# Optimization experiments

Measured on AMD Instinct MI355X. Metric: run time of the kernel, lower is better.

## Reference

```python
import jax, jax.numpy as jnp
import numpy as np

N_NODES = 50000
N_EDGES = 800000
ND = 64   # node_dim
HD = 128  # hidden_dim
ED = 32   # edge_dim


def setup_inputs() -> dict:
    key = jax.random.key(0)
    ks = jax.random.split(key, 16)
    init = lambda k, shape: (jax.random.normal(k, shape, jnp.float32)
                             / np.float32(np.sqrt(shape[0])))
    h = jax.random.normal(ks[0], (N_NODES, ND), jnp.float32)
    x = jax.random.normal(ks[1], (N_NODES, 3), jnp.float32) * 10.0
    edge_index = jax.random.randint(ks[2], (2, N_EDGES), 0, N_NODES, dtype=jnp.int64)
    # realistic edge distances = actual pairwise distances of sampled edges
    edge_dist = jnp.linalg.norm(x[edge_index[0]] - x[edge_index[1]], axis=-1)
    in_dim = 2 * ND + ED
    return {
        "h": h, "x": x, "edge_index": edge_index, "edge_dist": edge_dist,
        # edge_mlp: Linear(1, ED) -> SiLU -> Linear(ED, ED)
        "We1": init(ks[3], (1, ED)), "be1": jnp.zeros((ED,), jnp.float32),
        "We2": init(ks[4], (ED, ED)), "be2": jnp.zeros((ED,), jnp.float32),
        # node_mlp: Linear(in_dim, HD) -> SiLU -> Linear(HD, ND)
        "Wn1": init(ks[5], (in_dim, HD)), "bn1": jnp.zeros((HD,), jnp.float32),
        "Wn2": init(ks[6], (HD, ND)), "bn2": jnp.zeros((ND,), jnp.float32),
        # coord_mlp: Linear(in_dim, HD) -> SiLU -> Linear(HD, 1, bias=False)
        "Wc1": init(ks[7], (in_dim, HD)), "bc1": jnp.zeros((HD,), jnp.float32),
        "Wc2": init(ks[8], (HD, 1)),
    }


def reference(h, x, edge_index, edge_dist,
              We1, be1, We2, be2,
              Wn1, bn1, Wn2, bn2,
              Wc1, bc1, Wc2):
    n = h.shape[0]
    src, dst = edge_index[0], edge_index[1]
    # edge_mlp on scalar distance -> [E, ED]
    e = jax.nn.silu(edge_dist[:, None] @ We1 + be1) @ We2 + be2
    # gather + concat -> [E, 2*ND + ED]
    m_input = jnp.concatenate([h[src], h[dst], e], axis=-1)
    # node messages [E, ND]
    m = jax.nn.silu(m_input @ Wn1 + bn1) @ Wn2 + bn2
    h_agg = jax.ops.segment_sum(m, dst, num_segments=n)
    # coord update weight [E, 1]
    coord_weight = jax.nn.silu(m_input @ Wc1 + bc1) @ Wc2
    dir_vec = x[src] - x[dst]
    dir_len = jnp.clip(jnp.linalg.norm(dir_vec, axis=-1, keepdims=True), 1e-8)
    coord_update = coord_weight * (dir_vec / dir_len)
    x_agg = jax.ops.segment_sum(coord_update, dst, num_segments=n)
    return h + h_agg, x + x_agg
```

## Files before the change

### kernel.cpp

```cpp
#include <hip/hip_runtime.h>


#define NN 50000
#define NE 800000
#define NDIM 64
#define HDIM 128
#define NTILES (NE / 64)
#define MSTRIDE 168
#define HSTRIDE 136
#define NH (NN * NDIM)
#define NX (NN * 3)

#define WS_HBF    0
#define WS_WN1P   6400000
#define WS_WC1P   6440960
#define WS_BN1P   6481920
#define WS_BC1P   6482432

typedef __bf16 bf16x8 __attribute__((ext_vector_type(8)));
typedef float f32x4 __attribute__((ext_vector_type(4)));
typedef unsigned short ushort8 __attribute__((ext_vector_type(8)));
typedef unsigned short ushort4v __attribute__((ext_vector_type(4)));

__device__ __forceinline__ unsigned short f2bf(float f) {
    union { float f; unsigned int u; } c; c.f = f;
    unsigned int r = c.u + 0x7fffu + ((c.u >> 16) & 1u);
    return (unsigned short)(r >> 16);
}
__device__ __forceinline__ unsigned int pk2bf(float a, float b) {
    return (unsigned int)f2bf(a) | ((unsigned int)f2bf(b) << 16);
}
__device__ __forceinline__ float silu(float v) {
    return v * __builtin_amdgcn_rcpf(1.0f + __expf(-v));
}
__device__ __forceinline__ bf16x8 ld_frag(const unsigned short* p) {
    union { ushort8 u; bf16x8 v; } c;
    c.u = *(const ushort8*)p;
    return c.v;
}
__device__ __forceinline__ bf16x8 mk_frag(const unsigned short* u) {
    union { ushort8 uu; bf16x8 v; } c;
#pragma unroll
    for (int j = 0; j < 8; ++j) c.uu[j] = u[j];
    return c.v;
}

__global__ void init_out(const float* __restrict__ h, const float* __restrict__ x,
                         float* __restrict__ out) {
    int i = blockIdx.x * 256 + threadIdx.x;
    if (i < NH) out[i] = h[i];
    else if (i < NH + NX) out[i] = x[i - NH];
}

__global__ void prep_h(const float* __restrict__ h, unsigned short* __restrict__ hbf) {
    int i = (blockIdx.x * 256 + threadIdx.x) * 4;
    if (i < NH) {
        float4 v = *(const float4*)(h + i);
        ushort4v u = { f2bf(v.x), f2bf(v.y), f2bf(v.z), f2bf(v.w) };
        *(ushort4v*)(hbf + i) = u;
    }
}

__global__ void prep_w(const float* __restrict__ We2, const float* __restrict__ be2,
                       const float* __restrict__ Wn1, const float* __restrict__ bn1,
                       const float* __restrict__ Wc1, const float* __restrict__ bc1,
                       unsigned short* __restrict__ wn1p, unsigned short* __restrict__ wc1p,
                       float* __restrict__ bn1p, float* __restrict__ bc1p) {
    int idx = blockIdx.x * 256 + threadIdx.x;
    if (idx >= 160 * 128) return;
    int k = idx >> 7, n = idx & 127;
    float vn, vc;
    if (k < 128) {
        vn = Wn1[k * HDIM + n];
        vc = Wc1[k * HDIM + n];
    } else {
        int i = k - 128;
        float sn = 0.0f, sc = 0.0f;
        for (int j = 0; j < 32; ++j) {
            float w = We2[i * 32 + j];
            sn += w * Wn1[(128 + j) * HDIM + n];
            sc += w * Wc1[(128 + j) * HDIM + n];
        }
        vn = sn; vc = sc;
    }
    wn1p[idx] = f2bf(vn);
    wc1p[idx] = f2bf(vc);
    if (idx < 128) {
        float sn = bn1[idx], sc = bc1[idx];
        for (int j = 0; j < 32; ++j) {
            sn += be2[j] * Wn1[(128 + j) * HDIM + idx];
            sc += be2[j] * Wc1[(128 + j) * HDIM + idx];
        }
        bn1p[idx] = sn;
        bc1p[idx] = sc;
    }
}

__global__ __launch_bounds__(256, 2) void egnn_edges(
    const unsigned short* __restrict__ hbf, const float* __restrict__ x,
    const int* __restrict__ srcg, const int* __restrict__ dstg,
    const float* __restrict__ dist,
    const float* __restrict__ We1, const float* __restrict__ be1,
    const unsigned short* __restrict__ wn1p, const float* __restrict__ bn1p,
    const float* __restrict__ Wn2, const float* __restrict__ bn2,
    const unsigned short* __restrict__ wc1p, const float* __restrict__ bc1p,
    const float* __restrict__ Wc2,
    float* __restrict__ outh, float* __restrict__ outx) {

    __shared__ __align__(16) unsigned short mlds[64 * MSTRIDE];
    __shared__ __align__(16) unsigned short hl[64 * HSTRIDE];
    __shared__ int src_l[64];
    __shared__ int dst_l[64];
    __shared__ float dist_l[64];
    __shared__ float part_l[256];

    const int tid  = threadIdx.x;
    const int w    = tid >> 6;
    const int lane = tid & 63;
    const int l15  = lane & 15;
    const int quad = lane >> 4;

    bf16x8 wn1f[5][2], wc1f[5][2];
#pragma unroll
    for (int kc = 0; kc < 5; ++kc) {
#pragma unroll
        for (int nt = 0; nt < 2; ++nt) {
            unsigned short un[8], uc[8];
            const int n = w * 32 + l15 * 2 + nt;
#pragma unroll
            for (int j = 0; j < 8; ++j) {
                const int k = kc * 32 + quad * 8 + j;
                un[j] = wn1p[k * HDIM + n];
                uc[j] = wc1p[k * HDIM + n];
            }
            wn1f[kc][nt] = mk_frag(un);
            wc1f[kc][nt] = mk_frag(uc);
        }
    }
    bf16x8 wn2f[4];
#pragma unroll
    for (int kc = 0; kc < 4; ++kc) {
        unsigned short u[8];
        const int n = w * 16 + l15;
#pragma unroll
        for (int j = 0; j < 8; ++j) {
            const int k = kc * 32 + quad * 8 + j;
            u[j] = f2bf(Wn2[k * NDIM + n]);
        }
        wn2f[kc] = mk_frag(u);
    }
    const float biasN0 = bn1p[w * 32 + l15 * 2];
    const float biasN1 = bn1p[w * 32 + l15 * 2 + 1];
    const float biasC0 = bc1p[w * 32 + l15 * 2];
    const float biasC1 = bc1p[w * 32 + l15 * 2 + 1];
    const float bias2v = bn2[w * 16 + l15];
    const float wc2a = Wc2[w * 32 + l15 * 2];
    const float wc2b = Wc2[w * 32 + l15 * 2 + 1];

    for (int tile = blockIdx.x; tile < NTILES; tile += gridDim.x) {
        __syncthreads();

        if (tid < 64) {
            const int e = tile * 64 + tid;
            src_l[tid] = srcg[e];
            dst_l[tid] = dstg[e];
            dist_l[tid] = dist[e];
        }
        __syncthreads();

        {
            const int c8 = tid & 7, sub = tid >> 3;
#pragma unroll
            for (int it = 0; it < 2; ++it) {
                const int el = sub + it * 32;
                const ushort8 hs = *(const ushort8*)(hbf + (size_t)src_l[el] * NDIM + c8 * 8);
                const ushort8 hd = *(const ushort8*)(hbf + (size_t)dst_l[el] * NDIM + c8 * 8);
                *(ushort8*)&mlds[el * MSTRIDE + c8 * 8] = hs;
                *(ushort8*)&mlds[el * MSTRIDE + 64 + c8 * 8] = hd;
            }
        }
        {
            const float dv = dist_l[lane];
            ushort8 su;
#pragma unroll
            for (int j = 0; j < 8; ++j) {
                const int k = w * 8 + j;
                su[j] = f2bf(silu(fmaf(dv, We1[k], be1[k])));
            }
            *(ushort8*)&mlds[lane * MSTRIDE + 128 + w * 8] = su;
        }
        __syncthreads();

        f32x4 accN[4][2], accC[4][2];
#pragma unroll
        for (int mt = 0; mt < 4; ++mt) {
            accN[mt][0] = (f32x4){biasN0, biasN0, biasN0, biasN0};
            accN[mt][1] = (f32x4){biasN1, biasN1, biasN1, biasN1};
            accC[mt][0] = (f32x4){biasC0, biasC0, biasC0, biasC0};
            accC[mt][1] = (f32x4){biasC1, biasC1, biasC1, biasC1};
        }
#pragma unroll
        for (int kc = 0; kc < 5; ++kc) {
            bf16x8 af[4];
#pragma unroll
            for (int mt = 0; mt < 4; ++mt)
                af[mt] = ld_frag(&mlds[(mt * 16 + l15) * MSTRIDE + kc * 32 + quad * 8]);
#pragma unroll
            for (int mt = 0; mt < 4; ++mt) {
#pragma unroll
                for (int nt = 0; nt < 2; ++nt) {
                    accN[mt][nt] = __builtin_amdgcn_mfma_f32_16x16x32_bf16(
                        af[mt], wn1f[kc][nt], accN[mt][nt], 0, 0, 0);
                    accC[mt][nt] = __builtin_amdgcn_mfma_f32_16x16x32_bf16(
                        af[mt], wc1f[kc][nt], accC[mt][nt], 0, 0, 0);
                }
            }
        }

#pragma unroll
        for (int mt = 0; mt < 4; ++mt) {
#pragma unroll
            for (int r = 0; r < 4; ++r) {
                const int row = mt * 16 + quad * 4 + r;
                *(unsigned int*)&hl[row * HSTRIDE + w * 32 + l15 * 2] =
                    pk2bf(silu(accN[mt][0][r]), silu(accN[mt][1][r]));
            }
        }
        __syncthreads();

        f32x4 acc2[4];
#pragma unroll
        for (int mt = 0; mt < 4; ++mt) acc2[mt] = (f32x4){bias2v, bias2v, bias2v, bias2v};
#pragma unroll
        for (int kc = 0; kc < 4; ++kc) {
#pragma unroll
            for (int mt = 0; mt < 4; ++mt) {
                bf16x8 a2 = ld_frag(&hl[(mt * 16 + l15) * HSTRIDE + kc * 32 + quad * 8]);
                acc2[mt] = __builtin_amdgcn_mfma_f32_16x16x32_bf16(a2, wn2f[kc], acc2[mt], 0, 0, 0);
            }
        }
#pragma unroll
        for (int mt = 0; mt < 4; ++mt) {
#pragma unroll
            for (int r = 0; r < 4; ++r) {
                const int el = mt * 16 + quad * 4 + r;
                atomicAdd(outh + (size_t)dst_l[el] * NDIM + w * 16 + l15, acc2[mt][r]);
            }
        }

        {
            float vals[16];
#pragma unroll
            for (int mt = 0; mt < 4; ++mt)
#pragma unroll
                for (int r = 0; r < 4; ++r)
                    vals[mt * 4 + r] = silu(accC[mt][0][r]) * wc2a +
                                       silu(accC[mt][1][r]) * wc2b;
#pragma unroll
            for (int m = 8; m >= 1; m >>= 1) {
                const bool up = (l15 & m) != 0;
#pragma unroll
                for (int j = 0; j < 8; ++j) {
                    if (j < m) {
                        float send = up ? vals[j] : vals[j + m];
                        float recv = __shfl_xor(send, m, 64);
                        vals[j] = (up ? vals[j + m] : vals[j]) + recv;
                    }
                }
            }
            const int edge = ((l15 >> 2) << 4) + (quad << 2) + (l15 & 3);
            part_l[w * 64 + edge] = vals[0];
        }
        __syncthreads();

        if (tid < 64) {
            const float cw = part_l[tid] + part_l[64 + tid] + part_l[128 + tid] + part_l[192 + tid];
            const int sn = src_l[tid], dn = dst_l[tid];
            const float dx = x[sn * 3 + 0] - x[dn * 3 + 0];
            const float dy = x[sn * 3 + 1] - x[dn * 3 + 1];
            const float dz = x[sn * 3 + 2] - x[dn * 3 + 2];
            float len = sqrtf(dx * dx + dy * dy + dz * dz);
            len = fmaxf(len, 1e-8f);
            const float f = cw / len;
            atomicAdd(outx + (size_t)dn * 3 + 0, f * dx);
            atomicAdd(outx + (size_t)dn * 3 + 1, f * dy);
            atomicAdd(outx + (size_t)dn * 3 + 2, f * dz);
        }
    }
}

extern "C" void kernel_launch(void* const* d_in, const int* in_sizes, int n_in,
                              void* d_out, int out_size, void* d_ws, size_t ws_size,
                              hipStream_t stream) {
    const float* h    = (const float*)d_in[0];
    const float* x    = (const float*)d_in[1];
    const int*   ei   = (const int*)d_in[2];
    const float* dist = (const float*)d_in[3];
    const float* We1  = (const float*)d_in[4];
    const float* be1  = (const float*)d_in[5];
    const float* We2  = (const float*)d_in[6];
    const float* be2  = (const float*)d_in[7];
    const float* Wn1  = (const float*)d_in[8];
    const float* bn1  = (const float*)d_in[9];
    const float* Wn2  = (const float*)d_in[10];
    const float* bn2  = (const float*)d_in[11];
    const float* Wc1  = (const float*)d_in[12];
    const float* bc1  = (const float*)d_in[13];
    const float* Wc2  = (const float*)d_in[14];

    unsigned short* hbf  = (unsigned short*)((char*)d_ws + WS_HBF);
    unsigned short* wn1p = (unsigned short*)((char*)d_ws + WS_WN1P);
    unsigned short* wc1p = (unsigned short*)((char*)d_ws + WS_WC1P);
    float* bn1p = (float*)((char*)d_ws + WS_BN1P);
    float* bc1p = (float*)((char*)d_ws + WS_BC1P);

    float* outh = (float*)d_out;
    float* outx = outh + (size_t)NH;

    prep_h<<<(NH / 4 + 255) / 256, 256, 0, stream>>>(h, hbf);
    prep_w<<<(160 * 128 + 255) / 256, 256, 0, stream>>>(We2, be2, Wn1, bn1, Wc1, bc1,
                                                        wn1p, wc1p, bn1p, bc1p);
    init_out<<<(NH + NX + 255) / 256, 256, 0, stream>>>(h, x, (float*)d_out);
    egnn_edges<<<512, 256, 0, stream>>>(hbf, x, ei, ei + NE, dist,
                                        We1, be1, wn1p, bn1p,
                                        Wn2, bn2, wc1p, bc1p, Wc2,
                                        outh, outx);
}
```

Before: 450.1 us.

## Double-buffer edge tiles, prefetch next gathers, fuse prep kernels, drop coord reduction barrier

Merges the three prep kernels into one launch that copies h/x to the output and converts h to bf16 in the same pass. The edge kernel now double-buffers the LDS message tile, issuing the next tile's index, distance and h gathers during the current tile's MFMA work, and replaces __syncthreads with a raw lgkmcnt wait plus barrier. Unit direction vectors are precomputed one tile ahead, and each wave atomically adds its partial coordinate contribution directly instead of reducing through LDS. This trades extra LDS, registers and four times as many coord atomics for fewer barriers and hidden gather latency.

Result: slower. 810.3 us (+80.0%).

```diff
diff --git a/kernel.cpp b/kernel.cpp
--- a/kernel.cpp
+++ b/kernel.cpp
@@ -11,17 +11,19 @@
 #define NH (NN * NDIM)
 #define NX (NN * 3)
 
-#define WS_HBF    0
-#define WS_WN1P   6400000
-#define WS_WC1P   6440960
-#define WS_BN1P   6481920
-#define WS_BC1P   6482432
+#define WS_HBF   0
+#define WS_WN1P  6400000
+#define WS_WC1P  6440960
+#define WS_BN1P  6481920
+#define WS_BC1P  6482432
 
 typedef __bf16 bf16x8 __attribute__((ext_vector_type(8)));
 typedef float f32x4 __attribute__((ext_vector_type(4)));
 typedef unsigned short ushort8 __attribute__((ext_vector_type(8)));
 typedef unsigned short ushort4v __attribute__((ext_vector_type(4)));
 
+#define LGKM_BARRIER() asm volatile("s_waitcnt lgkmcnt(0)\n\ts_barrier" ::: "memory")
+
 __device__ __forceinline__ unsigned short f2bf(float f) {
     union { float f; unsigned int u; } c; c.f = f;
     unsigned int r = c.u + 0x7fffu + ((c.u >> 16) & 1u);
@@ -45,54 +47,52 @@
     return c.v;
 }
 
-__global__ void init_out(const float* __restrict__ h, const float* __restrict__ x,
-                         float* __restrict__ out) {
-    int i = blockIdx.x * 256 + threadIdx.x;
-    if (i < NH) out[i] = h[i];
-    else if (i < NH + NX) out[i] = x[i - NH];
-}
-
-__global__ void prep_h(const float* __restrict__ h, unsigned short* __restrict__ hbf) {
-    int i = (blockIdx.x * 256 + threadIdx.x) * 4;
-    if (i < NH) {
-        float4 v = *(const float4*)(h + i);
-        ushort4v u = { f2bf(v.x), f2bf(v.y), f2bf(v.z), f2bf(v.w) };
-        *(ushort4v*)(hbf + i) = u;
-    }
-}
-
-__global__ void prep_w(const float* __restrict__ We2, const float* __restrict__ be2,
-                       const float* __restrict__ Wn1, const float* __restrict__ bn1,
-                       const float* __restrict__ Wc1, const float* __restrict__ bc1,
-                       unsigned short* __restrict__ wn1p, unsigned short* __restrict__ wc1p,
-                       float* __restrict__ bn1p, float* __restrict__ bc1p) {
-    int idx = blockIdx.x * 256 + threadIdx.x;
-    if (idx >= 160 * 128) return;
-    int k = idx >> 7, n = idx & 127;
-    float vn, vc;
-    if (k < 128) {
-        vn = Wn1[k * HDIM + n];
-        vc = Wc1[k * HDIM + n];
-    } else {
-        int i = k - 128;
-        float sn = 0.0f, sc = 0.0f;
-        for (int j = 0; j < 32; ++j) {
-            float w = We2[i * 32 + j];
-            sn += w * Wn1[(128 + j) * HDIM + n];
-            sc += w * Wc1[(128 + j) * HDIM + n];
-        }
-        vn = sn; vc = sc;
-    }
-    wn1p[idx] = f2bf(vn);
-    wc1p[idx] = f2bf(vc);
-    if (idx < 128) {
-        float sn = bn1[idx], sc = bc1[idx];
-        for (int j = 0; j < 32; ++j) {
-            sn += be2[j] * Wn1[(128 + j) * HDIM + idx];
-            sc += be2[j] * Wc1[(128 + j) * HDIM + idx];
-        }
-        bn1p[idx] = sn;
-        bc1p[idx] = sc;
+__global__ void prep_all(
+    const float* __restrict__ h, const float* __restrict__ x,
+    const float* __restrict__ We2, const float* __restrict__ be2,
+    const float* __restrict__ Wn1, const float* __restrict__ bn1,
+    const float* __restrict__ Wc1, const float* __restrict__ bc1,
+    float* __restrict__ out, unsigned short* __restrict__ hbf,
+    unsigned short* __restrict__ wn1p, unsigned short* __restrict__ wc1p,
+    float* __restrict__ bn1p, float* __restrict__ bc1p) {
+    int gid = blockIdx.x * 256 + threadIdx.x;
+    if (gid < 837500) {
+        if (gid < 800000) {
+            float4 v = ((const float4*)h)[gid];
+            ((float4*)out)[gid] = v;
+            ushort4v u = { f2bf(v.x), f2bf(v.y), f2bf(v.z), f2bf(v.w) };
+            ((ushort4v*)hbf)[gid] = u;
+        } else {
+            ((float4*)out)[gid] = ((const float4*)x)[gid - 800000];
+        }
+    } else if (gid < 837500 + 20480) {
+        int idx = gid - 837500;
+        int k = idx >> 7, n = idx & 127;
+        float vn, vc;
+        if (k < 128) {
+            vn = Wn1[k * HDIM + n];
+            vc = Wc1[k * HDIM + n];
+        } else {
+            int i = k - 128;
+            float sn = 0.0f, sc = 0.0f;
+            for (int j = 0; j < 32; ++j) {
+                float wv = We2[i * 32 + j];
+                sn += wv * Wn1[(128 + j) * HDIM + n];
+                sc += wv * Wc1[(128 + j) * HDIM + n];
+            }
+            vn = sn; vc = sc;
+        }
+        wn1p[idx] = f2bf(vn);
+        wc1p[idx] = f2bf(vc);
+        if (idx < 128) {
+            float sn = bn1[idx], sc = bc1[idx];
+            for (int j = 0; j < 32; ++j) {
+                sn += be2[j] * Wn1[(128 + j) * HDIM + idx];
+                sc += be2[j] * Wc1[(128 + j) * HDIM + idx];
+            }
+            bn1p[idx] = sn;
+            bc1p[idx] = sc;
+        }
     }
 }
 
@@ -107,34 +107,35 @@
     const float* __restrict__ Wc2,
     float* __restrict__ outh, float* __restrict__ outx) {
 
-    __shared__ __align__(16) unsigned short mlds[64 * MSTRIDE];
+    __shared__ __align__(16) unsigned short mlds[2][64 * MSTRIDE];
     __shared__ __align__(16) unsigned short hl[64 * HSTRIDE];
-    __shared__ int src_l[64];
-    __shared__ int dst_l[64];
-    __shared__ float dist_l[64];
-    __shared__ float part_l[256];
+    __shared__ int dst_l[2][64];
+    __shared__ float4 unit_l[2][64];
 
     const int tid  = threadIdx.x;
     const int w    = tid >> 6;
     const int lane = tid & 63;
     const int l15  = lane & 15;
     const int quad = lane >> 4;
+    const int c8   = tid & 7;
+    const int sub  = tid >> 3;
+    const int bedge = ((l15 >> 2) << 4) + (quad << 2) + (l15 & 3);
 
     bf16x8 wn1f[5][2], wc1f[5][2];
 #pragma unroll
     for (int kc = 0; kc < 5; ++kc) {
 #pragma unroll
         for (int nt = 0; nt < 2; ++nt) {
-            unsigned short un[8], uc[8];
+            unsigned short un_[8], uc_[8];
             const int n = w * 32 + l15 * 2 + nt;
 #pragma unroll
             for (int j = 0; j < 8; ++j) {
                 const int k = kc * 32 + quad * 8 + j;
-                un[j] = wn1p[k * HDIM + n];
-                uc[j] = wc1p[k * HDIM + n];
-            }
-            wn1f[kc][nt] = mk_frag(un);
-            wc1f[kc][nt] = mk_frag(uc);
+                un_[j] = wn1p[k * HDIM + n];
+                uc_[j] = wc1p[k * HDIM + n];
+            }
+            wn1f[kc][nt] = mk_frag(un_);
+            wc1f[kc][nt] = mk_frag(uc_);
         }
     }
     bf16x8 wn2f[4];
@@ -148,6 +149,12 @@
             u[j] = f2bf(Wn2[k * NDIM + n]);
         }
         wn2f[kc] = mk_frag(u);
+    }
+    float we1r[8], be1r[8];
+#pragma unroll
+    for (int j = 0; j < 8; ++j) {
+        we1r[j] = We1[w * 8 + j];
+        be1r[j] = be1[w * 8 + j];
     }
     const float biasN0 = bn1p[w * 32 + l15 * 2];
     const float biasN1 = bn1p[w * 32 + l15 * 2 + 1];
@@ -157,39 +164,46 @@
     const float wc2a = Wc2[w * 32 + l15 * 2];
     const float wc2b = Wc2[w * 32 + l15 * 2 + 1];
 
-    for (int tile = blockIdx.x; tile < NTILES; tile += gridDim.x) {
-        __syncthreads();
-
+    const int t0 = blockIdx.x;
+    const int gstep = (int)gridDim.x;
+    {
+        const int sA = srcg[t0 * 64 + sub], sB = srcg[t0 * 64 + sub + 32];
+        const int dA = dstg[t0 * 64 + sub], dB = dstg[t0 * 64 + sub + 32];
+        const float dv = dist[t0 * 64 + lane];
+        const ushort8 hsa = *(const ushort8*)(hbf + sA * NDIM + c8 * 8);
+        const ushort8 hda = *(const ushort8*)(hbf + dA * NDIM + c8 * 8);
+        const ushort8 hsb = *(const ushort8*)(hbf + sB * NDIM + c8 * 8);
+        const ushort8 hdb = *(const ushort8*)(hbf + dB * NDIM + c8 * 8);
+        *(ushort8*)&mlds[0][sub * MSTRIDE + c8 * 8] = hsa;
+        *(ushort8*)&mlds[0][sub * MSTRIDE + 64 + c8 * 8] = hda;
+        *(ushort8*)&mlds[0][(sub + 32) * MSTRIDE + c8 * 8] = hsb;
+        *(ushort8*)&mlds[0][(sub + 32) * MSTRIDE + 64 + c8 * 8] = hdb;
+        ushort8 su;
+#pragma unroll
+        for (int j = 0; j < 8; ++j)
+            su[j] = f2bf(silu(fmaf(dv, we1r[j], be1r[j])));
+        *(ushort8*)&mlds[0][lane * MSTRIDE + 128 + w * 8] = su;
+        if (c8 == 0) { dst_l[0][sub] = dA; dst_l[0][sub + 32] = dB; }
         if (tid < 64) {
-            const int e = tile * 64 + tid;
-            src_l[tid] = srcg[e];
-            dst_l[tid] = dstg[e];
-            dist_l[tid] = dist[e];
-        }
-        __syncthreads();
-
-        {
-            const int c8 = tid & 7, sub = tid >> 3;
-#pragma unroll
-            for (int it = 0; it < 2; ++it) {
-                const int el = sub + it * 32;
-                const ushort8 hs = *(const ushort8*)(hbf + (size_t)src_l[el] * NDIM + c8 * 8);
-                const ushort8 hd = *(const ushort8*)(hbf + (size_t)dst_l[el] * NDIM + c8 * 8);
-                *(ushort8*)&mlds[el * MSTRIDE + c8 * 8] = hs;
-                *(ushort8*)&mlds[el * MSTRIDE + 64 + c8 * 8] = hd;
-            }
-        }
-        {
-            const float dv = dist_l[lane];
-            ushort8 su;
-#pragma unroll
-            for (int j = 0; j < 8; ++j) {
-                const int k = w * 8 + j;
-                su[j] = f2bf(silu(fmaf(dv, We1[k], be1[k])));
-            }
-            *(ushort8*)&mlds[lane * MSTRIDE + 128 + w * 8] = su;
-        }
-        __syncthreads();
+            const int us = srcg[t0 * 64 + tid], ud = dstg[t0 * 64 + tid];
+            const float ddx = x[us * 3 + 0] - x[ud * 3 + 0];
+            const float ddy = x[us * 3 + 1] - x[ud * 3 + 1];
+            const float ddz = x[us * 3 + 2] - x[ud * 3 + 2];
+            const float len = fmaxf(sqrtf(ddx * ddx + ddy * ddy + ddz * ddz), 1e-8f);
+            const float inv = __builtin_amdgcn_rcpf(len);
+            unit_l[0][tid] = make_float4(ddx * inv, ddy * inv, ddz * inv, 0.0f);
+        }
+    }
+
+    int p = 0;
+    for (int tile = t0; tile < NTILES; tile += gstep) {
+        const int tnx = tile + gstep;
+        const int tc = (tnx < NTILES) ? tnx : tile;
+        const int nsA = srcg[tc * 64 + sub], nsB = srcg[tc * 64 + sub + 32];
+        const int ndA = dstg[tc * 64 + sub], ndB = dstg[tc * 64 + sub + 32];
+        const float ndv = dist[tc * 64 + lane];
+
+        LGKM_BARRIER();
 
         f32x4 accN[4][2], accC[4][2];
 #pragma unroll
@@ -204,7 +218,7 @@
             bf16x8 af[4];
 #pragma unroll
             for (int mt = 0; mt < 4; ++mt)
-                af[mt] = ld_frag(&mlds[(mt * 16 + l15) * MSTRIDE + kc * 32 + quad * 8]);
+                af[mt] = ld_frag(&mlds[p][(mt * 16 + l15) * MSTRIDE + kc * 32 + quad * 8]);
 #pragma unroll
             for (int mt = 0; mt < 4; ++mt) {
 #pragma unroll
@@ -217,6 +231,11 @@
             }
         }
 
+        const ushort8 ghsa = *(const ushort8*)(hbf + nsA * NDIM + c8 * 8);
+        const ushort8 ghda = *(const ushort8*)(hbf + ndA * NDIM + c8 * 8);
+        const ushort8 ghsb = *(const ushort8*)(hbf + nsB * NDIM + c8 * 8);
+        const ushort8 ghdb = *(const ushort8*)(hbf + ndB * NDIM + c8 * 8);
+
 #pragma unroll
         for (int mt = 0; mt < 4; ++mt) {
 #pragma unroll
@@ -226,7 +245,7 @@
                     pk2bf(silu(accN[mt][0][r]), silu(accN[mt][1][r]));
             }
         }
-        __syncthreads();
+        LGKM_BARRIER();
 
         f32x4 acc2[4];
 #pragma unroll
@@ -244,7 +263,7 @@
 #pragma unroll
             for (int r = 0; r < 4; ++r) {
                 const int el = mt * 16 + quad * 4 + r;
-                atomicAdd(outh + (size_t)dst_l[el] * NDIM + w * 16 + l15, acc2[mt][r]);
+                atomicAdd(outh + dst_l[p][el] * NDIM + w * 16 + l15, acc2[mt][r]);
             }
         }
 
@@ -268,24 +287,36 @@
                     }
                 }
             }
-            const int edge = ((l15 >> 2) << 4) + (quad << 2) + (l15 & 3);
-            part_l[w * 64 + edge] = vals[0];
-        }
-        __syncthreads();
-
+            const float4 un = unit_l[p][bedge];
+            const int dn = dst_l[p][bedge];
+            const float cwp = vals[0];
+            atomicAdd(outx + dn * 3 + 0, cwp * un.x);
+            atomicAdd(outx + dn * 3 + 1, cwp * un.y);
+            atomicAdd(outx + dn * 3 + 2, cwp * un.z);
+        }
+
+        *(ushort8*)&mlds[p ^ 1][sub * MSTRIDE + c8 * 8] = ghsa;
+        *(ushort8*)&mlds[p ^ 1][sub * MSTRIDE + 64 + c8 * 8] = ghda;
+        *(ushort8*)&mlds[p ^ 1][(sub + 32) * MSTRIDE + c8 * 8] = ghsb;
+        *(ushort8*)&mlds[p ^ 1][(sub + 32) * MSTRIDE + 64 + c8 * 8] = ghdb;
+        {
+            ushort8 su;
+#pragma unroll
+            for (int j = 0; j < 8; ++j)
+                su[j] = f2bf(silu(fmaf(ndv, we1r[j], be1r[j])));
+            *(ushort8*)&mlds[p ^ 1][lane * MSTRIDE + 128 + w * 8] = su;
+        }
+        if (c8 == 0) { dst_l[p ^ 1][sub] = ndA; dst_l[p ^ 1][sub + 32] = ndB; }
         if (tid < 64) {
-            const float cw = part_l[tid] + part_l[64 + tid] + part_l[128 + tid] + part_l[192 + tid];
-            const int sn = src_l[tid], dn = dst_l[tid];
-            const float dx = x[sn * 3 + 0] - x[dn * 3 + 0];
-            const float dy = x[sn * 3 + 1] - x[dn * 3 + 1];
-            const float dz = x[sn * 3 + 2] - x[dn * 3 + 2];
-            float len = sqrtf(dx * dx + dy * dy + dz * dz);
-            len = fmaxf(len, 1e-8f);
-            const float f = cw / len;
-            atomicAdd(outx + (size_t)dn * 3 + 0, f * dx);
-            atomicAdd(outx + (size_t)dn * 3 + 1, f * dy);
-            atomicAdd(outx + (size_t)dn * 3 + 2, f * dz);
-        }
+            const int us = srcg[tc * 64 + tid], ud = dstg[tc * 64 + tid];
+            const float ddx = x[us * 3 + 0] - x[ud * 3 + 0];
+            const float ddy = x[us * 3 + 1] - x[ud * 3 + 1];
+            const float ddz = x[us * 3 + 2] - x[ud * 3 + 2];
+            const float len = fmaxf(sqrtf(ddx * ddx + ddy * ddy + ddz * ddz), 1e-8f);
+            const float inv = __builtin_amdgcn_rcpf(len);
+            unit_l[p ^ 1][tid] = make_float4(ddx * inv, ddy * inv, ddz * inv, 0.0f);
+        }
+        p ^= 1;
     }
 }
 
@@ -317,10 +348,10 @@
     float* outh = (float*)d_out;
     float* outx = outh + (size_t)NH;
 
-    prep_h<<<(NH / 4 + 255) / 256, 256, 0, stream>>>(h, hbf);
-    prep_w<<<(160 * 128 + 255) / 256, 256, 0, stream>>>(We2, be2, Wn1, bn1, Wc1, bc1,
-                                                        wn1p, wc1p, bn1p, bc1p);
-    init_out<<<(NH + NX + 255) / 256, 256, 0, stream>>>(h, x, (float*)d_out);
+    const int prep_items = 837500 + 20480;
+    prep_all<<<(prep_items + 255) / 256, 256, 0, stream>>>(
+        h, x, We2, be2, Wn1, bn1, Wc1, bc1,
+        (float*)d_out, hbf, wn1p, wc1p, bn1p, bc1p);
     egnn_edges<<<512, 256, 0, stream>>>(hbf, x, ei, ei + NE, dist,
                                         We1, be1, wn1p, bn1p,
                                         Wn2, bn2, wc1p, bc1p, Wc2,
```

## Bucket edges by destination and reduce messages in shared memory

Applied to the files above, without the earlier changes.

Adds a counting-sort pipeline (histogram, single-block scan, scatter) that groups edges into buckets of 16 destination nodes. The edge kernel then processes one bucket per block iteration and accumulates node and coordinate messages in shared-memory atomics, writing each node's result once instead of issuing global float atomics per edge. The three prep kernels are also merged into one, and We1/be1 are hoisted into registers. The cost is extra prep passes over all edges, global atomics in the scatter, and partially filled 64-edge tiles at bucket ends. Because the scatter order is nondeterministic, the summation order, and so the floating-point results, can vary slightly between runs.

After: 811.2 us. 80.2% more time.

```diff
diff --git a/kernel.cpp b/kernel.cpp
--- a/kernel.cpp
+++ b/kernel.cpp
@@ -5,17 +5,22 @@
 #define NE 800000
 #define NDIM 64
 #define HDIM 128
-#define NTILES (NE / 64)
+#define NBUCK 3125
 #define MSTRIDE 168
 #define HSTRIDE 136
 #define NH (NN * NDIM)
 #define NX (NN * 3)
 
 #define WS_HBF    0
-#define WS_WN1P   6400000
-#define WS_WC1P   6440960
-#define WS_BN1P   6481920
-#define WS_BC1P   6482432
+#define WS_SRCS   6400000
+#define WS_DSTS   9600000
+#define WS_DISTS  12800000
+#define WS_WN1P   16000000
+#define WS_WC1P   16040960
+#define WS_BN1P   16081920
+#define WS_BC1P   16082432
+#define WS_START  16082944
+#define WS_CURS   16095448
 
 typedef __bf16 bf16x8 __attribute__((ext_vector_type(8)));
 typedef float f32x4 __attribute__((ext_vector_type(4)));
@@ -45,61 +50,105 @@
     return c.v;
 }
 
-__global__ void init_out(const float* __restrict__ h, const float* __restrict__ x,
-                         float* __restrict__ out) {
-    int i = blockIdx.x * 256 + threadIdx.x;
-    if (i < NH) out[i] = h[i];
-    else if (i < NH + NX) out[i] = x[i - NH];
-}
-
-__global__ void prep_h(const float* __restrict__ h, unsigned short* __restrict__ hbf) {
-    int i = (blockIdx.x * 256 + threadIdx.x) * 4;
-    if (i < NH) {
-        float4 v = *(const float4*)(h + i);
-        ushort4v u = { f2bf(v.x), f2bf(v.y), f2bf(v.z), f2bf(v.w) };
-        *(ushort4v*)(hbf + i) = u;
-    }
-}
-
-__global__ void prep_w(const float* __restrict__ We2, const float* __restrict__ be2,
-                       const float* __restrict__ Wn1, const float* __restrict__ bn1,
-                       const float* __restrict__ Wc1, const float* __restrict__ bc1,
-                       unsigned short* __restrict__ wn1p, unsigned short* __restrict__ wc1p,
-                       float* __restrict__ bn1p, float* __restrict__ bc1p) {
-    int idx = blockIdx.x * 256 + threadIdx.x;
-    if (idx >= 160 * 128) return;
-    int k = idx >> 7, n = idx & 127;
-    float vn, vc;
-    if (k < 128) {
-        vn = Wn1[k * HDIM + n];
-        vc = Wc1[k * HDIM + n];
-    } else {
-        int i = k - 128;
-        float sn = 0.0f, sc = 0.0f;
-        for (int j = 0; j < 32; ++j) {
-            float w = We2[i * 32 + j];
-            sn += w * Wn1[(128 + j) * HDIM + n];
-            sc += w * Wc1[(128 + j) * HDIM + n];
-        }
-        vn = sn; vc = sc;
-    }
-    wn1p[idx] = f2bf(vn);
-    wc1p[idx] = f2bf(vc);
-    if (idx < 128) {
-        float sn = bn1[idx], sc = bc1[idx];
-        for (int j = 0; j < 32; ++j) {
-            sn += be2[j] * Wn1[(128 + j) * HDIM + idx];
-            sc += be2[j] * Wc1[(128 + j) * HDIM + idx];
-        }
-        bn1p[idx] = sn;
-        bc1p[idx] = sc;
+__global__ void prep_all(
+    const float* __restrict__ h, const float* __restrict__ x,
+    const float* __restrict__ We2, const float* __restrict__ be2,
+    const float* __restrict__ Wn1, const float* __restrict__ bn1,
+    const float* __restrict__ Wc1, const float* __restrict__ bc1,
+    float* __restrict__ out, unsigned short* __restrict__ hbf,
+    unsigned short* __restrict__ wn1p, unsigned short* __restrict__ wc1p,
+    float* __restrict__ bn1p, float* __restrict__ bc1p, int* __restrict__ hist) {
+    int gid = blockIdx.x * 256 + threadIdx.x;
+    if (gid < 837500) {
+        if (gid < 800000) {
+            float4 v = ((const float4*)h)[gid];
+            ((float4*)out)[gid] = v;
+            ushort4v u = { f2bf(v.x), f2bf(v.y), f2bf(v.z), f2bf(v.w) };
+            ((ushort4v*)hbf)[gid] = u;
+        } else {
+            ((float4*)out)[gid] = ((const float4*)x)[gid - 800000];
+        }
+    } else if (gid < 837500 + 20480) {
+        int idx = gid - 837500;
+        int k = idx >> 7, n = idx & 127;
+        float vn, vc;
+        if (k < 128) {
+            vn = Wn1[k * HDIM + n];
+            vc = Wc1[k * HDIM + n];
+        } else {
+            int i = k - 128;
+            float sn = 0.0f, sc = 0.0f;
+            for (int j = 0; j < 32; ++j) {
+                float wv = We2[i * 32 + j];
+                sn += wv * Wn1[(128 + j) * HDIM + n];
+                sc += wv * Wc1[(128 + j) * HDIM + n];
+            }
+            vn = sn; vc = sc;
+        }
+        wn1p[idx] = f2bf(vn);
+        wc1p[idx] = f2bf(vc);
+        if (idx < 128) {
+            float sn = bn1[idx], sc = bc1[idx];
+            for (int j = 0; j < 32; ++j) {
+                sn += be2[j] * Wn1[(128 + j) * HDIM + idx];
+                sc += be2[j] * Wc1[(128 + j) * HDIM + idx];
+            }
+            bn1p[idx] = sn;
+            bc1p[idx] = sc;
+        }
+    } else if (gid < 837500 + 20480 + NBUCK + 1) {
+        hist[gid - (837500 + 20480)] = 0;
+    }
+}
+
+__global__ void prep_hist(const int* __restrict__ dstg, int* __restrict__ hist) {
+    int e = blockIdx.x * 256 + threadIdx.x;
+    if (e < NE) atomicAdd(&hist[dstg[e] >> 4], 1);
+}
+
+__global__ void prep_scan(int* curs, int* start) {
+    __shared__ int sd[256];
+    __shared__ int carry_s;
+    const int tid = threadIdx.x;
+    if (tid == 0) carry_s = 0;
+    __syncthreads();
+    for (int c = 0; c < 13; ++c) {
+        const int i = c * 256 + tid;
+        const int v = (i < NBUCK) ? curs[i] : 0;
+        sd[tid] = v;
+        __syncthreads();
+        for (int off = 1; off < 256; off <<= 1) {
+            int t = (tid >= off) ? sd[tid - off] : 0;
+            __syncthreads();
+            sd[tid] += t;
+            __syncthreads();
+        }
+        const int excl = sd[tid] - v + carry_s;
+        if (i <= NBUCK) { start[i] = excl; curs[i] = excl; }
+        __syncthreads();
+        if (tid == 0) carry_s += sd[255];
+        __syncthreads();
+    }
+}
+
+__global__ void prep_scatter(const int* __restrict__ srcg, const int* __restrict__ dstg,
+                             const float* __restrict__ dist, int* __restrict__ curs,
+                             int* __restrict__ src_s, int* __restrict__ dst_s,
+                             float* __restrict__ dist_s) {
+    int e = blockIdx.x * 256 + threadIdx.x;
+    if (e < NE) {
+        int d = dstg[e];
+        int pos = atomicAdd(&curs[d >> 4], 1);
+        src_s[pos] = srcg[e];
+        dst_s[pos] = d;
+        dist_s[pos] = dist[e];
     }
 }
 
 __global__ __launch_bounds__(256, 2) void egnn_edges(
     const unsigned short* __restrict__ hbf, const float* __restrict__ x,
-    const int* __restrict__ srcg, const int* __restrict__ dstg,
-    const float* __restrict__ dist,
+    const int* __restrict__ src_s, const int* __restrict__ dst_s,
+    const float* __restrict__ dist_s, const int* __restrict__ start,
     const float* __restrict__ We1, const float* __restrict__ be1,
     const unsigned short* __restrict__ wn1p, const float* __restrict__ bn1p,
     const float* __restrict__ Wn2, const float* __restrict__ bn2,
@@ -109,6 +158,8 @@
 
     __shared__ __align__(16) unsigned short mlds[64 * MSTRIDE];
     __shared__ __align__(16) unsigned short hl[64 * HSTRIDE];
+    __shared__ __align__(16) float nodeacc[16][68];
+    __shared__ float xacc[16][3];
     __shared__ int src_l[64];
     __shared__ int dst_l[64];
     __shared__ float dist_l[64];
@@ -119,22 +170,23 @@
     const int lane = tid & 63;
     const int l15  = lane & 15;
     const int quad = lane >> 4;
+    const int bedge = ((l15 >> 2) << 4) + (quad << 2) + (l15 & 3);
 
     bf16x8 wn1f[5][2], wc1f[5][2];
 #pragma unroll
     for (int kc = 0; kc < 5; ++kc) {
 #pragma unroll
         for (int nt = 0; nt < 2; ++nt) {
-            unsigned short un[8], uc[8];
+            unsigned short un_[8], uc_[8];
             const int n = w * 32 + l15 * 2 + nt;
 #pragma unroll
             for (int j = 0; j < 8; ++j) {
                 const int k = kc * 32 + quad * 8 + j;
-                un[j] = wn1p[k * HDIM + n];
-                uc[j] = wc1p[k * HDIM + n];
-            }
-            wn1f[kc][nt] = mk_frag(un);
-            wc1f[kc][nt] = mk_frag(uc);
+                un_[j] = wn1p[k * HDIM + n];
+                uc_[j] = wc1p[k * HDIM + n];
+            }
+            wn1f[kc][nt] = mk_frag(un_);
+            wc1f[kc][nt] = mk_frag(uc_);
         }
     }
     bf16x8 wn2f[4];
@@ -148,6 +200,12 @@
             u[j] = f2bf(Wn2[k * NDIM + n]);
         }
         wn2f[kc] = mk_frag(u);
+    }
+    float we1r[8], be1r[8];
+#pragma unroll
+    for (int j = 0; j < 8; ++j) {
+        we1r[j] = We1[w * 8 + j];
+        be1r[j] = be1[w * 8 + j];
     }
     const float biasN0 = bn1p[w * 32 + l15 * 2];
     const float biasN1 = bn1p[w * 32 + l15 * 2 + 1];
@@ -157,135 +215,160 @@
     const float wc2a = Wc2[w * 32 + l15 * 2];
     const float wc2b = Wc2[w * 32 + l15 * 2 + 1];
 
-    for (int tile = blockIdx.x; tile < NTILES; tile += gridDim.x) {
+    for (int b = blockIdx.x; b < NBUCK; b += gridDim.x) {
+        const int base_node = b << 4;
+        const int e_start = start[b];
+        const int e_end = start[b + 1];
+
+        for (int i = tid; i < 16 * 68; i += 256) ((float*)nodeacc)[i] = 0.0f;
+        if (tid < 48) ((float*)xacc)[tid] = 0.0f;
+
+        for (int e0 = e_start; e0 < e_end; e0 += 64) {
+            const int cnt = min(64, e_end - e0);
+            __syncthreads();
+
+            if (tid < 64) {
+                const int ee = e0 + ((tid < cnt) ? tid : (cnt - 1));
+                src_l[tid] = src_s[ee];
+                dst_l[tid] = dst_s[ee];
+                dist_l[tid] = dist_s[ee];
+            }
+            __syncthreads();
+
+            {
+                const int c8 = tid & 7, sub = tid >> 3;
+#pragma unroll
+                for (int it = 0; it < 2; ++it) {
+                    const int el = sub + it * 32;
+                    const ushort8 hs = *(const ushort8*)(hbf + src_l[el] * NDIM + c8 * 8);
+                    const ushort8 hd = *(const ushort8*)(hbf + dst_l[el] * NDIM + c8 * 8);
+                    *(ushort8*)&mlds[el * MSTRIDE + c8 * 8] = hs;
+                    *(ushort8*)&mlds[el * MSTRIDE + 64 + c8 * 8] = hd;
+                }
+            }
+            {
+                const float dv = dist_l[lane];
+                ushort8 su;
+#pragma unroll
+                for (int j = 0; j < 8; ++j)
+                    su[j] = f2bf(silu(fmaf(dv, we1r[j], be1r[j])));
+                *(ushort8*)&mlds[lane * MSTRIDE + 128 + w * 8] = su;
+            }
+            __syncthreads();
+
+            f32x4 accN[4][2], accC[4][2];
+#pragma unroll
+            for (int mt = 0; mt < 4; ++mt) {
+                accN[mt][0] = (f32x4){biasN0, biasN0, biasN0, biasN0};
+                accN[mt][1] = (f32x4){biasN1, biasN1, biasN1, biasN1};
+                accC[mt][0] = (f32x4){biasC0, biasC0, biasC0, biasC0};
+                accC[mt][1] = (f32x4){biasC1, biasC1, biasC1, biasC1};
+            }
+#pragma unroll
+            for (int kc = 0; kc < 5; ++kc) {
+                bf16x8 af[4];
+#pragma unroll
+                for (int mt = 0; mt < 4; ++mt)
+                    af[mt] = ld_frag(&mlds[(mt * 16 + l15) * MSTRIDE + kc * 32 + quad * 8]);
+#pragma unroll
+                for (int mt = 0; mt < 4; ++mt) {
+#pragma unroll
+                    for (int nt = 0; nt < 2; ++nt) {
+                        accN[mt][nt] = __builtin_amdgcn_mfma_f32_16x16x32_bf16(
+                            af[mt], wn1f[kc][nt], accN[mt][nt], 0, 0, 0);
+                        accC[mt][nt] = __builtin_amdgcn_mfma_f32_16x16x32_bf16(
+                            af[mt], wc1f[kc][nt], accC[mt][nt], 0, 0, 0);
+                    }
+                }
+            }
+
+#pragma unroll
+            for (int mt = 0; mt < 4; ++mt) {
+#pragma unroll
+                for (int r = 0; r < 4; ++r) {
+                    const int row = mt * 16 + quad * 4 + r;
+                    *(unsigned int*)&hl[row * HSTRIDE + w * 32 + l15 * 2] =
+                        pk2bf(silu(accN[mt][0][r]), silu(accN[mt][1][r]));
+                }
+            }
+            __syncthreads();
+
+            f32x4 acc2[4];
+#pragma unroll
+            for (int mt = 0; mt < 4; ++mt) acc2[mt] = (f32x4){bias2v, bias2v, bias2v, bias2v};
+#pragma unroll
+            for (int kc = 0; kc < 4; ++kc) {
+#pragma unroll
+                for (int mt = 0; mt < 4; ++mt) {
+                    bf16x8 a2 = ld_frag(&hl[(mt * 16 + l15) * HSTRIDE + kc * 32 + quad * 8]);
+                    acc2[mt] = __builtin_amdgcn_mfma_f32_16x16x32_bf16(a2, wn2f[kc], acc2[mt], 0, 0, 0);
+                }
+            }
+#pragma unroll
+            for (int mt = 0; mt < 4; ++mt) {
+#pragma unroll
+                for (int r = 0; r < 4; ++r) {
+                    const int el = mt * 16 + quad * 4 + r;
+                    if (el < cnt)
+                        atomicAdd(&nodeacc[dst_l[el] - base_node][w * 16 + l15], acc2[mt][r]);
+                }
+            }
+
+            {
+                float vals[16];
+#pragma unroll
+                for (int mt = 0; mt < 4; ++mt)
+#pragma unroll
+                    for (int r = 0; r < 4; ++r)
+                        vals[mt * 4 + r] = silu(accC[mt][0][r]) * wc2a +
+                                           silu(accC[mt][1][r]) * wc2b;
+#pragma unroll
+                for (int m = 8; m >= 1; m >>= 1) {
+                    const bool up = (l15 & m) != 0;
+#pragma unroll
+                    for (int j = 0; j < 8; ++j) {
+                        if (j < m) {
+                            float send = up ? vals[j] : vals[j + m];
+                            float recv = __shfl_xor(send, m, 64);
+                            vals[j] = (up ? vals[j + m] : vals[j]) + recv;
+                        }
+                    }
+                }
+                part_l[w * 64 + bedge] = vals[0];
+            }
+            __syncthreads();
+
+            if (tid < cnt) {
+                const float cw = part_l[tid] + part_l[64 + tid] + part_l[128 + tid] + part_l[192 + tid];
+                const int sn = src_l[tid], dn = dst_l[tid];
+                const float dx = x[sn * 3 + 0] - x[dn * 3 + 0];
+                const float dy = x[sn * 3 + 1] - x[dn * 3 + 1];
+                const float dz = x[sn * 3 + 2] - x[dn * 3 + 2];
+                float len = sqrtf(dx * dx + dy * dy + dz * dz);
+                len = fmaxf(len, 1e-8f);
+                const float f = cw / len;
+                const int rel = dn - base_node;
+                atomicAdd(&xacc[rel][0], f * dx);
+                atomicAdd(&xacc[rel][1], f * dy);
+                atomicAdd(&xacc[rel][2], f * dz);
+            }
+        }
         __syncthreads();
 
-        if (tid < 64) {
-            const int e = tile * 64 + tid;
-            src_l[tid] = srcg[e];
-            dst_l[tid] = dstg[e];
-            dist_l[tid] = dist[e];
+        {
+            const int node = tid >> 4;
+            const int c4 = (tid & 15) * 4;
+            const float4 add = *(const float4*)&nodeacc[node][c4];
+            float* op = outh + (base_node + node) * NDIM + c4;
+            float4 cur = *(const float4*)op;
+            cur.x += add.x; cur.y += add.y; cur.z += add.z; cur.w += add.w;
+            *(float4*)op = cur;
+        }
+        if (tid < 48) {
+            const int node = tid / 3, c = tid - node * 3;
+            outx[(base_node + node) * 3 + c] += xacc[node][c];
         }
         __syncthreads();
-
-        {
-            const int c8 = tid & 7, sub = tid >> 3;
-#pragma unroll
-            for (int it = 0; it < 2; ++it) {
-                const int el = sub + it * 32;
-                const ushort8 hs = *(const ushort8*)(hbf + (size_t)src_l[el] * NDIM + c8 * 8);
-                const ushort8 hd = *(const ushort8*)(hbf + (size_t)dst_l[el] * NDIM + c8 * 8);
-                *(ushort8*)&mlds[el * MSTRIDE + c8 * 8] = hs;
-                *(ushort8*)&mlds[el * MSTRIDE + 64 + c8 * 8] = hd;
-            }
-        }
-        {
-            const float dv = dist_l[lane];
-            ushort8 su;
-#pragma unroll
-            for (int j = 0; j < 8; ++j) {
-                const int k = w * 8 + j;
-                su[j] = f2bf(silu(fmaf(dv, We1[k], be1[k])));
-            }
-            *(ushort8*)&mlds[lane * MSTRIDE + 128 + w * 8] = su;
-        }
-        __syncthreads();
-
-        f32x4 accN[4][2], accC[4][2];
-#pragma unroll
-        for (int mt = 0; mt < 4; ++mt) {
-            accN[mt][0] = (f32x4){biasN0, biasN0, biasN0, biasN0};
-            accN[mt][1] = (f32x4){biasN1, biasN1, biasN1, biasN1};
-            accC[mt][0] = (f32x4){biasC0, biasC0, biasC0, biasC0};
-            accC[mt][1] = (f32x4){biasC1, biasC1, biasC1, biasC1};
-        }
-#pragma unroll
-        for (int kc = 0; kc < 5; ++kc) {
-            bf16x8 af[4];
-#pragma unroll
-            for (int mt = 0; mt < 4; ++mt)
-                af[mt] = ld_frag(&mlds[(mt * 16 + l15) * MSTRIDE + kc * 32 + quad * 8]);
-#pragma unroll
-            for (int mt = 0; mt < 4; ++mt) {
-#pragma unroll
-                for (int nt = 0; nt < 2; ++nt) {
-                    accN[mt][nt] = __builtin_amdgcn_mfma_f32_16x16x32_bf16(
-                        af[mt], wn1f[kc][nt], accN[mt][nt], 0, 0, 0);
-                    accC[mt][nt] = __builtin_amdgcn_mfma_f32_16x16x32_bf16(
-                        af[mt], wc1f[kc][nt], accC[mt][nt], 0, 0, 0);
-                }
-            }
-        }
-
-#pragma unroll
-        for (int mt = 0; mt < 4; ++mt) {
-#pragma unroll
-            for (int r = 0; r < 4; ++r) {
-                const int row = mt * 16 + quad * 4 + r;
-                *(unsigned int*)&hl[row * HSTRIDE + w * 32 + l15 * 2] =
-                    pk2bf(silu(accN[mt][0][r]), silu(accN[mt][1][r]));
-            }
-        }
-        __syncthreads();
-
-        f32x4 acc2[4];
-#pragma unroll
-        for (int mt = 0; mt < 4; ++mt) acc2[mt] = (f32x4){bias2v, bias2v, bias2v, bias2v};
-#pragma unroll
-        for (int kc = 0; kc < 4; ++kc) {
-#pragma unroll
-            for (int mt = 0; mt < 4; ++mt) {
-                bf16x8 a2 = ld_frag(&hl[(mt * 16 + l15) * HSTRIDE + kc * 32 + quad * 8]);
-                acc2[mt] = __builtin_amdgcn_mfma_f32_16x16x32_bf16(a2, wn2f[kc], acc2[mt], 0, 0, 0);
-            }
-        }
-#pragma unroll
-        for (int mt = 0; mt < 4; ++mt) {
-#pragma unroll
-            for (int r = 0; r < 4; ++r) {
-                const int el = mt * 16 + quad * 4 + r;
-                atomicAdd(outh + (size_t)dst_l[el] * NDIM + w * 16 + l15, acc2[mt][r]);
-            }
-        }
-
-        {
-            float vals[16];
-#pragma unroll
-            for (int mt = 0; mt < 4; ++mt)
-#pragma unroll
-                for (int r = 0; r < 4; ++r)
-                    vals[mt * 4 + r] = silu(accC[mt][0][r]) * wc2a +
-                                       silu(accC[mt][1][r]) * wc2b;
-#pragma unroll
-            for (int m = 8; m >= 1; m >>= 1) {
-                const bool up = (l15 & m) != 0;
-#pragma unroll
-                for (int j = 0; j < 8; ++j) {
-                    if (j < m) {
-                        float send = up ? vals[j] : vals[j + m];
-                        float recv = __shfl_xor(send, m, 64);
-                        vals[j] = (up ? vals[j + m] : vals[j]) + recv;
-                    }
-                }
-            }
-            const int edge = ((l15 >> 2) << 4) + (quad << 2) + (l15 & 3);
-            part_l[w * 64 + edge] = vals[0];
-        }
-        __syncthreads();
-
-        if (tid < 64) {
-            const float cw = part_l[tid] + part_l[64 + tid] + part_l[128 + tid] + part_l[192 + tid];
-            const int sn = src_l[tid], dn = dst_l[tid];
-            const float dx = x[sn * 3 + 0] - x[dn * 3 + 0];
-            const float dy = x[sn * 3 + 1] - x[dn * 3 + 1];
-            const float dz = x[sn * 3 + 2] - x[dn * 3 + 2];
-            float len = sqrtf(dx * dx + dy * dy + dz * dz);
-            len = fmaxf(len, 1e-8f);
-            const float f = cw / len;
-            atomicAdd(outx + (size_t)dn * 3 + 0, f * dx);
-            atomicAdd(outx + (size_t)dn * 3 + 1, f * dy);
-            atomicAdd(outx + (size_t)dn * 3 + 2, f * dz);
-        }
     }
 }
 
@@ -308,20 +391,29 @@
     const float* bc1  = (const float*)d_in[13];
     const float* Wc2  = (const float*)d_in[14];
 
-    unsigned short* hbf  = (unsigned short*)((char*)d_ws + WS_HBF);
-    unsigned short* wn1p = (unsigned short*)((char*)d_ws + WS_WN1P);
-    unsigned short* wc1p = (unsigned short*)((char*)d_ws + WS_WC1P);
-    float* bn1p = (float*)((char*)d_ws + WS_BN1P);
-    float* bc1p = (float*)((char*)d_ws + WS_BC1P);
+    unsigned short* hbf   = (unsigned short*)((char*)d_ws + WS_HBF);
+    int*            src_s = (int*)((char*)d_ws + WS_SRCS);
+    int*            dst_s = (int*)((char*)d_ws + WS_DSTS);
+    float*          dist_s= (float*)((char*)d_ws + WS_DISTS);
+    unsigned short* wn1p  = (unsigned short*)((char*)d_ws + WS_WN1P);
+    unsigned short* wc1p  = (unsigned short*)((char*)d_ws + WS_WC1P);
+    float* bn1p  = (float*)((char*)d_ws + WS_BN1P);
+    float* bc1p  = (float*)((char*)d_ws + WS_BC1P);
+    int*   startb= (int*)((char*)d_ws + WS_START);
+    int*   curs  = (int*)((char*)d_ws + WS_CURS);
 
     float* outh = (float*)d_out;
     float* outx = outh + (size_t)NH;
 
-    prep_h<<<(NH / 4 + 255) / 256, 256, 0, stream>>>(h, hbf);
-    prep_w<<<(160 * 128 + 255) / 256, 256, 0, stream>>>(We2, be2, Wn1, bn1, Wc1, bc1,
-                                                        wn1p, wc1p, bn1p, bc1p);
-    init_out<<<(NH + NX + 255) / 256, 256, 0, stream>>>(h, x, (float*)d_out);
-    egnn_edges<<<512, 256, 0, stream>>>(hbf, x, ei, ei + NE, dist,
+    const int prep_items = 837500 + 20480 + NBUCK + 1;
+    prep_all<<<(prep_items + 255) / 256, 256, 0, stream>>>(
+        h, x, We2, be2, Wn1, bn1, Wc1, bc1,
+        (float*)d_out, hbf, wn1p, wc1p, bn1p, bc1p, curs);
+    prep_hist<<<(NE + 255) / 256, 256, 0, stream>>>(ei + NE, curs);
+    prep_scan<<<1, 256, 0, stream>>>(curs, startb);
+    prep_scatter<<<(NE + 255) / 256, 256, 0, stream>>>(ei, ei + NE, dist, curs,
+                                                       src_s, dst_s, dist_s);
+    egnn_edges<<<512, 256, 0, stream>>>(hbf, x, src_s, dst_s, dist_s, startb,
                                         We1, be1, wn1p, bn1p,
                                         Wn2, bn2, wc1p, bc1p, Wc2,
                                         outh, outx);
```
